# Kernel tuning notes

Measured on AMD Instinct MI355X. Metric: run time of the kernel, lower is better.

## Reference

```python
import jax, jax.numpy as jnp
import numpy as np

H, HS, C = 16, 64, 1024  # num_heads, head_size, n_embd

def setup_inputs() -> dict:
    key = jax.random.key(0)
    ks = jax.random.split(key, 5)
    B, T = 2, 2048
    s = 1.0 / np.sqrt(C)
    return {
        "x": jax.random.normal(ks[0], (B, T, C), dtype=jnp.float32),
        "Wq": jax.random.normal(ks[1], (H, C, HS), dtype=jnp.float32) * s,
        "Wk": jax.random.normal(ks[2], (H, C, HS), dtype=jnp.float32) * s,
        "Wv": jax.random.normal(ks[3], (H, C, HS), dtype=jnp.float32) * s,
        "Wo": jax.random.normal(ks[4], (C, C), dtype=jnp.float32) * s,
    }

def reference(x, Wq, Wk, Wv, Wo):
    B, T, Cdim = x.shape
    scale = Cdim ** -0.5  # original scales by n_embd**-0.5, not head_size
    q = jnp.einsum('btc,hcd->bhtd', x, Wq)
    k = jnp.einsum('btc,hcd->bhtd', x, Wk)
    v = jnp.einsum('btc,hcd->bhtd', x, Wv)
    wei = jnp.einsum('bhtd,bhsd->bhts', q, k) * scale  # [B,H,T,T]
    causal = jnp.tril(jnp.ones((T, T), dtype=bool))
    wei = jnp.where(causal, wei, -jnp.inf)
    wei = jax.nn.softmax(wei, axis=-1)
    out = jnp.einsum('bhts,bhsd->bhtd', wei, v)  # [B,H,T,HS]
    out = out.transpose(0, 2, 1, 3).reshape(B, T, -1)  # concat heads -> [B,T,C]
    return out @ Wo.T
```

## Files before the change

kernel.cpp:

```cpp
#include <hip/hip_runtime.h>

typedef unsigned short ushort_t;
typedef __bf16 bf16x8 __attribute__((ext_vector_type(8)));
typedef float f32x4 __attribute__((ext_vector_type(4)));
typedef float f32x16 __attribute__((ext_vector_type(16)));
typedef unsigned short ushortx8 __attribute__((ext_vector_type(8)));
typedef unsigned int uintx4 __attribute__((ext_vector_type(4)));

#define NH 16
#define HS 64
#define CD 1024
#define NB 2
#define NT 2048
#define BT (NB * NT)
#define N3 (3 * CD)

#define L2E_DIV32 0.04508422002778011f


__device__ __forceinline__ ushort_t bf16_rne(float f) {
  union { float f; unsigned u; } v; v.f = f;
  unsigned u = v.u;
  unsigned r = (u + 0x7FFFu + ((u >> 16) & 1u)) >> 16;
  return (ushort_t)r;
}

__device__ __forceinline__ void gload_lds16(const ushort_t* g, ushort_t* l) {
  __builtin_amdgcn_global_load_lds(
      (const __attribute__((address_space(1))) unsigned int*)g,
      (__attribute__((address_space(3))) unsigned int*)l, 16, 0, 0);
}

__device__ __forceinline__ f32x4 mfma16(ushortx8 a, ushortx8 b, f32x4 c) {
  return __builtin_amdgcn_mfma_f32_16x16x32_bf16(
      __builtin_bit_cast(bf16x8, a), __builtin_bit_cast(bf16x8, b), c, 0, 0, 0);
}

__device__ __forceinline__ f32x16 mfma32(ushortx8 a, ushortx8 b, f32x16 c) {
  return __builtin_amdgcn_mfma_f32_32x32x16_bf16(
      __builtin_bit_cast(bf16x8, a), __builtin_bit_cast(bf16x8, b), c, 0, 0, 0);
}

__device__ __forceinline__ unsigned cvt_pk_bf16(float lo, float hi) {
  unsigned r;
  asm("v_cvt_pk_bf16_f32 %0, %1, %2" : "=v"(r) : "v"(lo), "v"(hi));
  return r;
}

__device__ __forceinline__ void plswap(unsigned &a, unsigned &b) {
  asm volatile("v_permlane32_swap_b32 %0, %1" : "+v"(a), "+v"(b));
}


__global__ __launch_bounds__(256)
void pack_cast(const float4* __restrict__ in, ushort_t* __restrict__ out, int n4) {
  const int i = blockIdx.x * 256 + threadIdx.x;
  if (i >= n4) return;
  const float4 v = in[i];
  ushort4 r;
  r.x = bf16_rne(v.x); r.y = bf16_rne(v.y);
  r.z = bf16_rne(v.z); r.w = bf16_rne(v.w);
  *(ushort4*)(out + (size_t)i * 4) = r;
}

__global__ __launch_bounds__(256)
void pack_wqkv(const float* __restrict__ Wq, const float* __restrict__ Wk,
               const float* __restrict__ Wv, ushort_t* __restrict__ out) {
  __shared__ ushort_t tile[64 * 66];
  const int sh = blockIdx.y;
  const int s = sh >> 4, h = sh & 15;
  const float* W = (s == 0) ? Wq : ((s == 1) ? Wk : Wv);
  const int c0 = blockIdx.x * 64;
  const int t = threadIdx.x;
#pragma unroll
  for (int j = 0; j < 16; ++j) {
    const int idx = t + j * 256;
    const int ci = idx >> 6, d = idx & 63;
    const float v = W[(size_t)(h * 1024 + c0 + ci) * 64 + d];
    tile[d * 66 + ci] = bf16_rne(v);
  }
  __syncthreads();
#pragma unroll
  for (int j = 0; j < 16; ++j) {
    const int idx = t + j * 256;
    const int d = idx >> 6, ci = idx & 63;
    out[(size_t)(s * 1024 + h * 64 + d) * 1024 + c0 + ci] = tile[d * 66 + ci];
  }
}


template <bool OUT_BF16>
__global__ __launch_bounds__(256)
void gemm_bt(const ushort_t* __restrict__ A, const ushort_t* __restrict__ Bt,
             void* __restrict__ Cv, int M, int N, int K) {
  __shared__ __align__(16) ushort_t ldsA[2][128 * 32];
  __shared__ __align__(16) ushort_t ldsB[2][128 * 32];
  const int tid = threadIdx.x;
  const int lane = tid & 63;
  const int wave = tid >> 6;
  const int row0 = blockIdx.y * 128;
  const int col0 = blockIdx.x * 128;
  const int wm = wave >> 1, wn = wave & 1;

  f32x4 acc[4][4] = {};

  const int ce = (tid & 3) * 8;

  auto stage = [&](int buf, int kt) {
    const int kbase = kt * 32;
#pragma unroll
    for (int j = 0; j < 2; ++j) {
      const int r = j * 64 + (tid >> 2);
      gload_lds16(A + (size_t)(row0 + r) * K + kbase + ce,
                  &ldsA[buf][(j * 256 + wave * 64) * 8]);
      gload_lds16(Bt + (size_t)(col0 + r) * K + kbase + ce,
                  &ldsB[buf][(j * 256 + wave * 64) * 8]);
    }
  };

  const int arow_off = (wm * 64 + (lane & 15)) * 32 + (lane >> 4) * 8;
  const int brow_off = (wn * 64 + (lane & 15)) * 32 + (lane >> 4) * 8;

  auto compute = [&](int buf) {
    ushortx8 af[4], bf[4];
#pragma unroll
    for (int m = 0; m < 4; ++m)
      af[m] = *(const ushortx8*)&ldsA[buf][arow_off + m * 512];
#pragma unroll
    for (int n = 0; n < 4; ++n)
      bf[n] = *(const ushortx8*)&ldsB[buf][brow_off + n * 512];
#pragma unroll
    for (int m = 0; m < 4; ++m)
#pragma unroll
      for (int n = 0; n < 4; ++n)
        acc[m][n] = mfma16(af[m], bf[n], acc[m][n]);
  };

  stage(0, 0);
  __syncthreads();
  const int nk = K >> 5;
  for (int kt = 0; kt < nk; ++kt) {
    const int cur = kt & 1;
    if (kt + 1 < nk) stage(cur ^ 1, kt + 1);
    compute(cur);
    __syncthreads();
  }

#pragma unroll
  for (int m = 0; m < 4; ++m) {
    const int rbase = row0 + wm * 64 + m * 16 + (lane >> 4) * 4;
#pragma unroll
    for (int n = 0; n < 4; ++n) {
      const int col = col0 + wn * 64 + n * 16 + (lane & 15);
#pragma unroll
      for (int i = 0; i < 4; ++i) {
        const size_t off = (size_t)(rbase + i) * N + col;
        if constexpr (OUT_BF16) ((ushort_t*)Cv)[off] = bf16_rne(acc[m][n][i]);
        else                    ((float*)Cv)[off]    = acc[m][n][i];
      }
    }
  }
}


__global__ __launch_bounds__(256, 2)
void attn_fwd2(const ushort_t* __restrict__ QKV, ushort_t* __restrict__ O) {
  __shared__ __align__(16) ushort_t Klds[2][64 * 64];
  __shared__ __align__(16) ushort_t Vlds[2][64 * 64];

  const int tid = threadIdx.x;
  const int lane = tid & 63;
  const int w = tid >> 6;
  const int l31 = lane & 31;
  const int h = lane >> 5;

  const int d0 = blockIdx.x;
  const int bh = (d0 & 7) + 8 * (d0 >> 7);
  const int qb = 15 - ((d0 >> 3) & 15);
  const int b = bh >> 4, head = bh & 15;
  const size_t base = (size_t)b * NT * N3;

  const int qw0 = qb * 128 + w * 32;
  const int qg = qw0 + l31;
  const int ntiles = 2 * qb + 2;
  const int tmax = 2 * qb + (w >> 1);

  ushortx8 qf[4];
  {
    const ushort_t* qp = QKV + base + (size_t)qg * N3 + head * 64 + h * 8;
#pragma unroll
    for (int kc = 0; kc < 4; ++kc)
      qf[kc] = *(const ushortx8*)(qp + kc * 16);
  }

  f32x16 oA = {}, oB = {};
  float m_r = -INFINITY, l_r = 0.f;

  const int vr = l31;
  const int vc = w * 2 + h;

  ushortx8 vst0, vst1;
  {
    const ushort_t* vp = QKV + base + (size_t)(2 * vr) * N3 + 2048 + head * 64 + vc * 8;
    vst0 = *(const ushortx8*)(vp);
    vst1 = *(const ushortx8*)(vp + N3);
  }
#pragma unroll
  for (int i = 0; i < 2; ++i) {
    const int ch = i * 256 + tid;
    const int row = ch >> 3, cc = ch & 7;
    gload_lds16(QKV + base + (size_t)row * N3 + 1024 + head * 64 + ((cc ^ (row & 7)) * 8),
                &Klds[0][(i * 256 + w * 64) * 8]);
  }
#pragma unroll
  for (int e = 0; e < 8; ++e) {
    const int d = vc * 8 + e;
    ushort2 val; val.x = vst0[e]; val.y = vst1[e];
    *(ushort2*)((char*)&Vlds[0][0] + d * 128 + (((vr >> 2) ^ (d & 7)) * 16) + 4 * (vr & 3)) = val;
  }
  asm volatile("s_waitcnt lgkmcnt(0)" ::: "memory");

  int curb = 0;
  for (int t = 0; t < ntiles; ++t) {
    const bool hasn = (t + 1 < ntiles);
    const int nxt = curb ^ 1;
    if (hasn) {
      const int key0n = (t + 1) * 64;
      const ushort_t* vp =
          QKV + base + (size_t)(key0n + 2 * vr) * N3 + 2048 + head * 64 + vc * 8;
      vst0 = *(const ushortx8*)(vp);
      vst1 = *(const ushortx8*)(vp + N3);
#pragma unroll
      for (int i = 0; i < 2; ++i) {
        const int ch = i * 256 + tid;
        const int row = ch >> 3, cc = ch & 7;
        gload_lds16(QKV + base + (size_t)(key0n + row) * N3 + 1024 + head * 64 +
                        ((cc ^ (row & 7)) * 8),
                    &Klds[nxt][(i * 256 + w * 64) * 8]);
      }
      asm volatile("s_waitcnt vmcnt(4)" ::: "memory");
    } else {
      asm volatile("s_waitcnt vmcnt(0)" ::: "memory");
    }
    __builtin_amdgcn_s_barrier();
    asm volatile("" ::: "memory");

    if (t <= tmax) {
      const int key0 = t * 64;
      f32x16 sA = {}, sB = {};
#pragma unroll
      for (int kc = 0; kc < 4; ++kc) {
        const int cc0 = ((2 * kc + h) ^ (l31 & 7)) * 8;
        const ushortx8 k0 = *(const ushortx8*)&Klds[curb][l31 * 64 + cc0];
        const ushortx8 k1 = *(const ushortx8*)&Klds[curb][(32 + l31) * 64 + cc0];
        sA = mfma32(k0, qf[kc], sA);
        sB = mfma32(k1, qf[kc], sB);
      }

      float s[32];
#pragma unroll
      for (int r = 0; r < 16; ++r) {
        s[r]      = sA[r] * L2E_DIV32;
        s[16 + r] = sB[r] * L2E_DIV32;
      }
      if (key0 + 63 > qw0) {
        const int kb0 = key0 + 4 * h;
#pragma unroll
        for (int r = 0; r < 16; ++r) {
          const int krow = (r & 3) + 8 * (r >> 2);
          if (kb0 + krow > qg)      s[r]      = -INFINITY;
          if (kb0 + 32 + krow > qg) s[16 + r] = -INFINITY;
        }
      }

      float mx = s[0];
#pragma unroll
      for (int r = 1; r < 32; ++r) mx = fmaxf(mx, s[r]);
      mx = fmaxf(mx, __shfl_xor(mx, 32, 64));
      const float mn = fmaxf(m_r, mx);
      const float alpha = exp2f(m_r - mn);
      m_r = mn;
      float rs = 0.f;
#pragma unroll
      for (int r = 0; r < 32; ++r) {
        s[r] = exp2f(s[r] - mn);
        rs += s[r];
      }
      rs += __shfl_xor(rs, 32, 64);
      l_r = l_r * alpha + rs;
#pragma unroll
      for (int r = 0; r < 16; ++r) { oA[r] *= alpha; oB[r] *= alpha; }

      unsigned u[16];
#pragma unroll
      for (int j = 0; j < 16; ++j) u[j] = cvt_pk_bf16(s[2 * j], s[2 * j + 1]);
      plswap(u[0], u[2]);   plswap(u[1], u[3]);
      plswap(u[4], u[6]);   plswap(u[5], u[7]);
      plswap(u[8], u[10]);  plswap(u[9], u[11]);
      plswap(u[12], u[14]); plswap(u[13], u[15]);

#pragma unroll
      for (int kc = 0; kc < 4; ++kc) {
        uintx4 pw;
        pw[0] = u[4 * kc + 0]; pw[1] = u[4 * kc + 1];
        pw[2] = u[4 * kc + 2]; pw[3] = u[4 * kc + 3];
        const ushortx8 pav = __builtin_bit_cast(ushortx8, pw);
        const int cc0 = ((2 * kc + h) ^ (l31 & 7)) * 8;
        const ushortx8 va = *(const ushortx8*)&Vlds[curb][l31 * 64 + cc0];
        const ushortx8 vb = *(const ushortx8*)&Vlds[curb][(32 + l31) * 64 + cc0];
        oA = mfma32(va, pav, oA);
        oB = mfma32(vb, pav, oB);
      }
    }

    if (hasn) {
#pragma unroll
      for (int e = 0; e < 8; ++e) {
        const int d = vc * 8 + e;
        ushort2 val; val.x = vst0[e]; val.y = vst1[e];
        *(ushort2*)((char*)&Vlds[nxt][0] + d * 128 + (((vr >> 2) ^ (d & 7)) * 16) +
                    4 * (vr & 3)) = val;
      }
    }
    asm volatile("s_waitcnt lgkmcnt(0)" ::: "memory");
    __builtin_amdgcn_s_barrier();
    asm volatile("" ::: "memory");
    curb ^= 1;
  }

  const float inv_l = 1.0f / l_r;
  ushort_t* op = O + ((size_t)(b * NT + qg)) * 1024 + head * 64;
#pragma unroll
  for (int db = 0; db < 2; ++db) {
#pragma unroll
    for (int g = 0; g < 4; ++g) {
      ushort4 pk;
      if (db == 0) {
        pk.x = bf16_rne(oA[4 * g + 0] * inv_l);
        pk.y = bf16_rne(oA[4 * g + 1] * inv_l);
        pk.z = bf16_rne(oA[4 * g + 2] * inv_l);
        pk.w = bf16_rne(oA[4 * g + 3] * inv_l);
      } else {
        pk.x = bf16_rne(oB[4 * g + 0] * inv_l);
        pk.y = bf16_rne(oB[4 * g + 1] * inv_l);
        pk.z = bf16_rne(oB[4 * g + 2] * inv_l);
        pk.w = bf16_rne(oB[4 * g + 3] * inv_l);
      }
      *(ushort4*)(op + db * 32 + 8 * g + 4 * h) = pk;
    }
  }
}


extern "C" void kernel_launch(void* const* d_in, const int* in_sizes, int n_in,
                              void* d_out, int out_size, void* d_ws, size_t ws_size,
                              hipStream_t stream) {
  (void)in_sizes; (void)n_in; (void)out_size; (void)ws_size;
  const float* x  = (const float*)d_in[0];
  const float* Wq = (const float*)d_in[1];
  const float* Wk = (const float*)d_in[2];
  const float* Wv = (const float*)d_in[3];
  const float* Wo = (const float*)d_in[4];

  char* ws = (char*)d_ws;
  ushort_t* Xbf    = (ushort_t*)(ws);
  ushort_t* Wqkv_t = (ushort_t*)(ws + 8388608);
  ushort_t* Wo_bf  = (ushort_t*)(ws + 14680064);
  ushort_t* QKV    = (ushort_t*)(ws + 16777216);
  ushort_t* Obf    = (ushort_t*)(ws + 41943040);

  pack_cast<<<4096, 256, 0, stream>>>((const float4*)x, Xbf, 1048576);
  pack_cast<<<1024, 256, 0, stream>>>((const float4*)Wo, Wo_bf, 262144);
  pack_wqkv<<<dim3(16, 48), 256, 0, stream>>>(Wq, Wk, Wv, Wqkv_t);

  gemm_bt<true><<<dim3(24, 32), 256, 0, stream>>>(Xbf, Wqkv_t, QKV, BT, N3, CD);
  attn_fwd2<<<dim3(512), 256, 0, stream>>>(QKV, Obf);
  gemm_bt<false><<<dim3(8, 32), 256, 0, stream>>>(Obf, Wo_bf, d_out, BT, CD, CD);
}
```

Baseline: 148.0 us.

## Drop LDS staging in attention: pre-transpose V, load K/V directly into registers

Adds a separate kernel that transposes V into a head-major [d, T] layout so that attention waves can load V fragments straight from global memory. The attention kernel drops the shared-memory double buffer and block barriers. Each wave now handles its own 32-query tile and register-prefetches the next K tile, skips the fully masked half of the diagonal tile, and only rescales the accumulator when the running max grows by more than a threshold. The cost is an extra kernel launch and transpose pass, redundant global/L2 K/V reads across waves in place of shared LDS reuse, and higher register pressure.

```diff
diff --git a/kernel.cpp b/kernel.cpp
--- a/kernel.cpp
+++ b/kernel.cpp
@@ -85,6 +85,35 @@
     const int idx = t + j * 256;
     const int d = idx >> 6, ci = idx & 63;
     out[(size_t)(s * 1024 + h * 64 + d) * 1024 + c0 + ci] = tile[d * 66 + ci];
+  }
+}
+
+__global__ __launch_bounds__(256)
+void vtrans(const ushort_t* __restrict__ QKV, ushort_t* __restrict__ Vt) {
+  __shared__ ushort_t tile[64 * 66];
+  const int bh = blockIdx.y;
+  const int b = bh >> 4, h = bh & 15;
+  const int t0 = blockIdx.x * 64;
+  const int tid = threadIdx.x;
+  const ushort_t* src = QKV + ((size_t)b * NT + t0) * N3 + 2048 + h * 64;
+#pragma unroll
+  for (int i = 0; i < 2; ++i) {
+    const int ch = i * 256 + tid;
+    const int r = ch >> 3, c8 = ch & 7;
+    const ushortx8 v = *(const ushortx8*)(src + (size_t)r * N3 + c8 * 8);
+#pragma unroll
+    for (int e = 0; e < 8; ++e) tile[(c8 * 8 + e) * 66 + r] = v[e];
+  }
+  __syncthreads();
+  ushort_t* dst = Vt + ((size_t)bh * 64) * NT + t0;
+#pragma unroll
+  for (int i = 0; i < 2; ++i) {
+    const int ch = i * 256 + tid;
+    const int d = ch >> 3, c8 = ch & 7;
+    ushortx8 o;
+#pragma unroll
+    for (int e = 0; e < 8; ++e) o[e] = tile[d * 66 + c8 * 8 + e];
+    *(ushortx8*)(dst + (size_t)d * NT + c8 * 8) = o;
   }
 }
 
@@ -164,168 +193,179 @@
 
 
 __global__ __launch_bounds__(256, 2)
-void attn_fwd2(const ushort_t* __restrict__ QKV, ushort_t* __restrict__ O) {
-  __shared__ __align__(16) ushort_t Klds[2][64 * 64];
-  __shared__ __align__(16) ushort_t Vlds[2][64 * 64];
-
+void attn_fwd3(const ushort_t* __restrict__ QKV, const ushort_t* __restrict__ Vt,
+               ushort_t* __restrict__ O) {
   const int tid = threadIdx.x;
+  const int w = tid >> 6;
   const int lane = tid & 63;
-  const int w = tid >> 6;
   const int l31 = lane & 31;
   const int h = lane >> 5;
 
-  const int d0 = blockIdx.x;
-  const int bh = (d0 & 7) + 8 * (d0 >> 7);
-  const int qb = 15 - ((d0 >> 3) & 15);
+  const int x = blockIdx.x;
+  const int bh = x & 31;
+  const int qt = (15 - (x >> 5)) * 4 + w;
   const int b = bh >> 4, head = bh & 15;
   const size_t base = (size_t)b * NT * N3;
-
-  const int qw0 = qb * 128 + w * 32;
-  const int qg = qw0 + l31;
-  const int ntiles = 2 * qb + 2;
-  const int tmax = 2 * qb + (w >> 1);
+  const int q0 = qt * 32;
+  const int qg = q0 + l31;
+  const int ntiles = (qt >> 1) + 1;
+  const bool oddq = (qt & 1) != 0;
+
+  const ushort_t* Kbase = QKV + base + 1024 + head * 64;
+  const ushort_t* Vbase = Vt + ((size_t)bh * 64) * NT;
 
   ushortx8 qf[4];
   {
     const ushort_t* qp = QKV + base + (size_t)qg * N3 + head * 64 + h * 8;
 #pragma unroll
-    for (int kc = 0; kc < 4; ++kc)
-      qf[kc] = *(const ushortx8*)(qp + kc * 16);
+    for (int kc = 0; kc < 4; ++kc) qf[kc] = *(const ushortx8*)(qp + kc * 16);
   }
 
   f32x16 oA = {}, oB = {};
   float m_r = -INFINITY, l_r = 0.f;
 
-  const int vr = l31;
-  const int vc = w * 2 + h;
-
-  ushortx8 vst0, vst1;
+  ushortx8 ka0[4], ka1[4], kb0[4], kb1[4];
+
   {
-    const ushort_t* vp = QKV + base + (size_t)(2 * vr) * N3 + 2048 + head * 64 + vc * 8;
-    vst0 = *(const ushortx8*)(vp);
-    vst1 = *(const ushortx8*)(vp + N3);
-  }
-#pragma unroll
-  for (int i = 0; i < 2; ++i) {
-    const int ch = i * 256 + tid;
-    const int row = ch >> 3, cc = ch & 7;
-    gload_lds16(QKV + base + (size_t)row * N3 + 1024 + head * 64 + ((cc ^ (row & 7)) * 8),
-                &Klds[0][(i * 256 + w * 64) * 8]);
-  }
-#pragma unroll
-  for (int e = 0; e < 8; ++e) {
-    const int d = vc * 8 + e;
-    ushort2 val; val.x = vst0[e]; val.y = vst1[e];
-    *(ushort2*)((char*)&Vlds[0][0] + d * 128 + (((vr >> 2) ^ (d & 7)) * 16) + 4 * (vr & 3)) = val;
-  }
-  asm volatile("s_waitcnt lgkmcnt(0)" ::: "memory");
-
-  int curb = 0;
-  for (int t = 0; t < ntiles; ++t) {
-    const bool hasn = (t + 1 < ntiles);
-    const int nxt = curb ^ 1;
-    if (hasn) {
-      const int key0n = (t + 1) * 64;
-      const ushort_t* vp =
-          QKV + base + (size_t)(key0n + 2 * vr) * N3 + 2048 + head * 64 + vc * 8;
-      vst0 = *(const ushortx8*)(vp);
-      vst1 = *(const ushortx8*)(vp + N3);
-#pragma unroll
-      for (int i = 0; i < 2; ++i) {
-        const int ch = i * 256 + tid;
-        const int row = ch >> 3, cc = ch & 7;
-        gload_lds16(QKV + base + (size_t)(key0n + row) * N3 + 1024 + head * 64 +
-                        ((cc ^ (row & 7)) * 8),
-                    &Klds[nxt][(i * 256 + w * 64) * 8]);
-      }
-      asm volatile("s_waitcnt vmcnt(4)" ::: "memory");
-    } else {
-      asm volatile("s_waitcnt vmcnt(0)" ::: "memory");
-    }
-    __builtin_amdgcn_s_barrier();
-    asm volatile("" ::: "memory");
-
-    if (t <= tmax) {
-      const int key0 = t * 64;
-      f32x16 sA = {}, sB = {};
-#pragma unroll
-      for (int kc = 0; kc < 4; ++kc) {
-        const int cc0 = ((2 * kc + h) ^ (l31 & 7)) * 8;
-        const ushortx8 k0 = *(const ushortx8*)&Klds[curb][l31 * 64 + cc0];
-        const ushortx8 k1 = *(const ushortx8*)&Klds[curb][(32 + l31) * 64 + cc0];
-        sA = mfma32(k0, qf[kc], sA);
-        sB = mfma32(k1, qf[kc], sB);
-      }
-
-      float s[32];
-#pragma unroll
-      for (int r = 0; r < 16; ++r) {
-        s[r]      = sA[r] * L2E_DIV32;
-        s[16 + r] = sB[r] * L2E_DIV32;
-      }
-      if (key0 + 63 > qw0) {
-        const int kb0 = key0 + 4 * h;
+    const bool hB0 = (ntiles == 1) && !oddq;
+#pragma unroll
+    for (int kc = 0; kc < 4; ++kc)
+      ka0[kc] = *(const ushortx8*)(Kbase + (size_t)l31 * N3 + kc * 16 + h * 8);
+    if (!hB0) {
+#pragma unroll
+      for (int kc = 0; kc < 4; ++kc)
+        ka1[kc] = *(const ushortx8*)(Kbase + (size_t)(32 + l31) * N3 + kc * 16 + h * 8);
+    }
+  }
+
+  auto step = [&](int t, ushortx8 (&kc0)[4], ushortx8 (&kc1)[4],
+                  ushortx8 (&kn0)[4], ushortx8 (&kn1)[4]) {
+    const int key0 = t * 64;
+    const bool last = (t == ntiles - 1);
+    const bool halfB = last && !oddq;
+
+    ushortx8 va[4], vb[4];
+#pragma unroll
+    for (int kc = 0; kc < 4; ++kc) {
+      if (kc < 2 || !halfB) {
+        va[kc] = *(const ushortx8*)(Vbase + (size_t)l31 * NT + key0 + kc * 16 + h * 8);
+        vb[kc] = *(const ushortx8*)(Vbase + (size_t)(32 + l31) * NT + key0 + kc * 16 + h * 8);
+      }
+    }
+    if (t + 1 < ntiles) {
+      const int nk0 = (t + 1) * 64;
+      const bool nhB = (t + 1 == ntiles - 1) && !oddq;
+#pragma unroll
+      for (int kc = 0; kc < 4; ++kc)
+        kn0[kc] = *(const ushortx8*)(Kbase + (size_t)(nk0 + l31) * N3 + kc * 16 + h * 8);
+      if (!nhB) {
+#pragma unroll
+        for (int kc = 0; kc < 4; ++kc)
+          kn1[kc] = *(const ushortx8*)(Kbase + (size_t)(nk0 + 32 + l31) * N3 + kc * 16 + h * 8);
+      }
+    }
+
+    f32x16 sA = {}, sB = {};
+#pragma unroll
+    for (int kc = 0; kc < 4; ++kc) sA = mfma32(kc0[kc], qf[kc], sA);
+    if (!halfB) {
+#pragma unroll
+      for (int kc = 0; kc < 4; ++kc) sB = mfma32(kc1[kc], qf[kc], sB);
+    }
+
+#pragma unroll
+    for (int r = 0; r < 16; ++r) sA[r] *= L2E_DIV32;
+    if (!halfB) {
+#pragma unroll
+      for (int r = 0; r < 16; ++r) sB[r] *= L2E_DIV32;
+    }
+    if (last) {
+      const int kb = key0 + 4 * h;
+      if (halfB) {
 #pragma unroll
         for (int r = 0; r < 16; ++r) {
           const int krow = (r & 3) + 8 * (r >> 2);
-          if (kb0 + krow > qg)      s[r]      = -INFINITY;
-          if (kb0 + 32 + krow > qg) s[16 + r] = -INFINITY;
+          if (kb + krow > qg) sA[r] = -INFINITY;
         }
-      }
-
-      float mx = s[0];
-#pragma unroll
-      for (int r = 1; r < 32; ++r) mx = fmaxf(mx, s[r]);
-      mx = fmaxf(mx, __shfl_xor(mx, 32, 64));
+      } else {
+#pragma unroll
+        for (int r = 0; r < 16; ++r) {
+          const int krow = (r & 3) + 8 * (r >> 2);
+          if (kb + 32 + krow > qg) sB[r] = -INFINITY;
+        }
+      }
+    }
+
+    float mm[16];
+    if (!halfB) {
+#pragma unroll
+      for (int r = 0; r < 16; ++r) mm[r] = fmaxf(sA[r], sB[r]);
+    } else {
+#pragma unroll
+      for (int r = 0; r < 16; ++r) mm[r] = sA[r];
+    }
+#pragma unroll
+    for (int st = 8; st >= 1; st >>= 1)
+#pragma unroll
+      for (int r = 0; r < st; ++r) mm[r] = fmaxf(mm[r], mm[r + st]);
+    float mx = fmaxf(mm[0], __shfl_xor(mm[0], 32, 64));
+
+    if (__any(mx > m_r + 8.0f)) {
       const float mn = fmaxf(m_r, mx);
       const float alpha = exp2f(m_r - mn);
       m_r = mn;
-      float rs = 0.f;
-#pragma unroll
-      for (int r = 0; r < 32; ++r) {
-        s[r] = exp2f(s[r] - mn);
-        rs += s[r];
-      }
-      rs += __shfl_xor(rs, 32, 64);
-      l_r = l_r * alpha + rs;
+      l_r *= alpha;
 #pragma unroll
       for (int r = 0; r < 16; ++r) { oA[r] *= alpha; oB[r] *= alpha; }
-
-      unsigned u[16];
-#pragma unroll
-      for (int j = 0; j < 16; ++j) u[j] = cvt_pk_bf16(s[2 * j], s[2 * j + 1]);
-      plswap(u[0], u[2]);   plswap(u[1], u[3]);
-      plswap(u[4], u[6]);   plswap(u[5], u[7]);
+    }
+
+    unsigned u[16];
+    float ps[8];
+#pragma unroll
+    for (int j = 0; j < 8; ++j) {
+      const float e0 = exp2f(sA[2 * j] - m_r);
+      const float e1 = exp2f(sA[2 * j + 1] - m_r);
+      u[j] = cvt_pk_bf16(e0, e1);
+      ps[j] = e0 + e1;
+    }
+    if (!halfB) {
+#pragma unroll
+      for (int j = 0; j < 8; ++j) {
+        const float e0 = exp2f(sB[2 * j] - m_r);
+        const float e1 = exp2f(sB[2 * j + 1] - m_r);
+        u[8 + j] = cvt_pk_bf16(e0, e1);
+        ps[j] += e0 + e1;
+      }
+    }
+#pragma unroll
+    for (int st = 4; st >= 1; st >>= 1)
+#pragma unroll
+      for (int r = 0; r < st; ++r) ps[r] += ps[r + st];
+    l_r += ps[0] + __shfl_xor(ps[0], 32, 64);
+
+    plswap(u[0], u[2]);   plswap(u[1], u[3]);
+    plswap(u[4], u[6]);   plswap(u[5], u[7]);
+    if (!halfB) {
       plswap(u[8], u[10]);  plswap(u[9], u[11]);
       plswap(u[12], u[14]); plswap(u[13], u[15]);
-
-#pragma unroll
-      for (int kc = 0; kc < 4; ++kc) {
+    }
+
+#pragma unroll
+    for (int kc = 0; kc < 4; ++kc) {
+      if (kc < 2 || !halfB) {
         uintx4 pw;
         pw[0] = u[4 * kc + 0]; pw[1] = u[4 * kc + 1];
         pw[2] = u[4 * kc + 2]; pw[3] = u[4 * kc + 3];
         const ushortx8 pav = __builtin_bit_cast(ushortx8, pw);
-        const int cc0 = ((2 * kc + h) ^ (l31 & 7)) * 8;
-        const ushortx8 va = *(const ushortx8*)&Vlds[curb][l31 * 64 + cc0];
-        const ushortx8 vb = *(const ushortx8*)&Vlds[curb][(32 + l31) * 64 + cc0];
-        oA = mfma32(va, pav, oA);
-        oB = mfma32(vb, pav, oB);
-      }
-    }
-
-    if (hasn) {
-#pragma unroll
-      for (int e = 0; e < 8; ++e) {
-        const int d = vc * 8 + e;
-        ushort2 val; val.x = vst0[e]; val.y = vst1[e];
-        *(ushort2*)((char*)&Vlds[nxt][0] + d * 128 + (((vr >> 2) ^ (d & 7)) * 16) +
-                    4 * (vr & 3)) = val;
-      }
-    }
-    asm volatile("s_waitcnt lgkmcnt(0)" ::: "memory");
-    __builtin_amdgcn_s_barrier();
-    asm volatile("" ::: "memory");
-    curb ^= 1;
+        oA = mfma32(va[kc], pav, oA);
+        oB = mfma32(vb[kc], pav, oB);
+      }
+    }
+  };
+
+  for (int t = 0; t < ntiles; t += 2) {
+    step(t, ka0, ka1, kb0, kb1);
+    if (t + 1 < ntiles) step(t + 1, kb0, kb1, ka0, ka1);
   }
 
   const float inv_l = 1.0f / l_r;
@@ -368,12 +408,14 @@
   ushort_t* Wo_bf  = (ushort_t*)(ws + 14680064);
   ushort_t* QKV    = (ushort_t*)(ws + 16777216);
   ushort_t* Obf    = (ushort_t*)(ws + 41943040);
+  ushort_t* Vt     = (ushort_t*)(ws + 50331648);
 
   pack_cast<<<4096, 256, 0, stream>>>((const float4*)x, Xbf, 1048576);
   pack_cast<<<1024, 256, 0, stream>>>((const float4*)Wo, Wo_bf, 262144);
   pack_wqkv<<<dim3(16, 48), 256, 0, stream>>>(Wq, Wk, Wv, Wqkv_t);
 
   gemm_bt<true><<<dim3(24, 32), 256, 0, stream>>>(Xbf, Wqkv_t, QKV, BT, N3, CD);
-  attn_fwd2<<<dim3(512), 256, 0, stream>>>(QKV, Obf);
+  vtrans<<<dim3(32, 32), 256, 0, stream>>>(QKV, Vt);
+  attn_fwd3<<<512, 256, 0, stream>>>(QKV, Vt, Obf);
   gemm_bt<false><<<dim3(8, 32), 256, 0, stream>>>(Obf, Wo_bf, d_out, BT, CD, CD);
 }
```

New measurement: 164.7 us. 11.3% more time.

## Split long causal attention rows across blocks with a separate merge kernel

Applied to the files above, without the earlier changes.

Attention for long query blocks is split into 2 to 4 key-range chunks per block (split-KV), giving 1280 blocks with partial outputs and row max/sum stored in workspace. A new merge kernel then combines the chunks. Other changes: the softmax scale moves into the QKV GEMM epilogue, the diagonal tile skips its masked half, online-softmax rescaling only happens when the max grows by more than 8, and occupancy hints rise to 4 blocks. The cost is an extra launch, workspace traffic, and bf16 rounding of partial outputs.

```diff
diff --git a/kernel.cpp b/kernel.cpp
--- a/kernel.cpp
+++ b/kernel.cpp
@@ -17,12 +17,20 @@
 
 #define L2E_DIV32 0.04508422002778011f
 
+#define PART1_OFF 50331648
+#define SLOT_BYTES 18432
+#define R0_SLOTS 796
+
 
 __device__ __forceinline__ ushort_t bf16_rne(float f) {
   union { float f; unsigned u; } v; v.f = f;
   unsigned u = v.u;
   unsigned r = (u + 0x7FFFu + ((u >> 16) & 1u)) >> 16;
   return (ushort_t)r;
+}
+
+__device__ __forceinline__ float bf2f(ushort_t u) {
+  union { unsigned u; float f; } v; v.u = ((unsigned)u) << 16; return v.f;
 }
 
 __device__ __forceinline__ void gload_lds16(const ushort_t* g, ushort_t* l) {
@@ -92,7 +100,7 @@
 template <bool OUT_BF16>
 __global__ __launch_bounds__(256)
 void gemm_bt(const ushort_t* __restrict__ A, const ushort_t* __restrict__ Bt,
-             void* __restrict__ Cv, int M, int N, int K) {
+             void* __restrict__ Cv, int M, int N, int K, int qcols) {
   __shared__ __align__(16) ushort_t ldsA[2][128 * 32];
   __shared__ __align__(16) ushort_t ldsB[2][128 * 32];
   const int tid = threadIdx.x;
@@ -101,6 +109,7 @@
   const int row0 = blockIdx.y * 128;
   const int col0 = blockIdx.x * 128;
   const int wm = wave >> 1, wn = wave & 1;
+  const float sc = (col0 < qcols) ? L2E_DIV32 : 1.0f;
 
   f32x4 acc[4][4] = {};
 
@@ -122,18 +131,18 @@
   const int brow_off = (wn * 64 + (lane & 15)) * 32 + (lane >> 4) * 8;
 
   auto compute = [&](int buf) {
-    ushortx8 af[4], bf[4];
+    ushortx8 af[4], bfr[4];
 #pragma unroll
     for (int m = 0; m < 4; ++m)
       af[m] = *(const ushortx8*)&ldsA[buf][arow_off + m * 512];
 #pragma unroll
     for (int n = 0; n < 4; ++n)
-      bf[n] = *(const ushortx8*)&ldsB[buf][brow_off + n * 512];
+      bfr[n] = *(const ushortx8*)&ldsB[buf][brow_off + n * 512];
 #pragma unroll
     for (int m = 0; m < 4; ++m)
 #pragma unroll
       for (int n = 0; n < 4; ++n)
-        acc[m][n] = mfma16(af[m], bf[n], acc[m][n]);
+        acc[m][n] = mfma16(af[m], bfr[n], acc[m][n]);
   };
 
   stage(0, 0);
@@ -155,16 +164,17 @@
 #pragma unroll
       for (int i = 0; i < 4; ++i) {
         const size_t off = (size_t)(rbase + i) * N + col;
-        if constexpr (OUT_BF16) ((ushort_t*)Cv)[off] = bf16_rne(acc[m][n][i]);
-        else                    ((float*)Cv)[off]    = acc[m][n][i];
-      }
-    }
-  }
-}
-
-
-__global__ __launch_bounds__(256, 2)
-void attn_fwd2(const ushort_t* __restrict__ QKV, ushort_t* __restrict__ O) {
+        if constexpr (OUT_BF16) ((ushort_t*)Cv)[off] = bf16_rne(acc[m][n][i] * sc);
+        else                    ((float*)Cv)[off]    = acc[m][n][i] * sc;
+      }
+    }
+  }
+}
+
+
+__global__ __launch_bounds__(256, 4)
+void attn_fwd4(const ushort_t* __restrict__ QKV, ushort_t* __restrict__ O,
+               char* __restrict__ wsb) {
   __shared__ __align__(16) ushort_t Klds[2][64 * 64];
   __shared__ __align__(16) ushort_t Vlds[2][64 * 64];
 
@@ -174,70 +184,76 @@
   const int l31 = lane & 31;
   const int h = lane >> 5;
 
-  const int d0 = blockIdx.x;
-  const int bh = (d0 & 7) + 8 * (d0 >> 7);
-  const int qb = 15 - ((d0 >> 3) & 15);
+  const int x = blockIdx.x;
+  const int bh = x & 31;
+  const int c = x >> 5;
+  int qb, j, k;
+  if (c < 16)      { qb = 12 + (c >> 2); j = c & 3; k = 4; }
+  else if (c < 28) { const int e = c - 16; const int q = e / 3; qb = 8 + q; j = e - q * 3; k = 3; }
+  else if (c < 36) { const int e = c - 28; qb = 4 + (e >> 1); j = e & 1; k = 2; }
+  else             { qb = c - 36; j = 0; k = 1; }
+  const int nt = 2 * qb + 2;
+  const int bsz = nt / k, rem = nt - bsz * k;
+  const int t0 = j * bsz + (j < rem ? j : rem);
+  const int t1 = t0 + bsz + (j < rem ? 1 : 0);
+  const bool lastc = (t1 == nt);
+
   const int b = bh >> 4, head = bh & 15;
   const size_t base = (size_t)b * NT * N3;
-
   const int qw0 = qb * 128 + w * 32;
   const int qg = qw0 + l31;
-  const int ntiles = 2 * qb + 2;
-  const int tmax = 2 * qb + (w >> 1);
+  const int tmax = lastc ? (2 * qb + (w >> 1)) : (t1 - 1);
 
   ushortx8 qf[4];
   {
     const ushort_t* qp = QKV + base + (size_t)qg * N3 + head * 64 + h * 8;
 #pragma unroll
-    for (int kc = 0; kc < 4; ++kc)
-      qf[kc] = *(const ushortx8*)(qp + kc * 16);
-  }
+    for (int kc = 0; kc < 4; ++kc) qf[kc] = *(const ushortx8*)(qp + kc * 16);
+  }
+
+  int koff[4];
+#pragma unroll
+  for (int kc = 0; kc < 4; ++kc)
+    koff[kc] = l31 * 128 + (((2 * kc + h) ^ (l31 & 7)) * 16);
+
+  const int vr = l31, vc = w * 2 + h;
+  int voff[8];
+#pragma unroll
+  for (int e = 0; e < 8; ++e)
+    voff[e] = (vc * 8 + e) * 128 + (((vr >> 2) ^ e) * 16) + 4 * (vr & 3);
+
+  const int rowA = tid >> 3, ccA = tid & 7;
+  const int rowB = 32 + rowA;
+  const ushort_t* kg = QKV + base + 1024 + head * 64;
+  const ushort_t* ksA = kg + (size_t)(t0 * 64 + rowA) * N3 + ((ccA ^ (rowA & 7)) * 8);
+  const ushort_t* ksB = kg + (size_t)(t0 * 64 + rowB) * N3 + ((ccA ^ (rowB & 7)) * 8);
+  const ushort_t* vs  = QKV + base + (size_t)(t0 * 64 + 2 * vr) * N3 + 2048 + head * 64 + vc * 8;
+  const size_t tadv = (size_t)64 * N3;
 
   f32x16 oA = {}, oB = {};
   float m_r = -INFINITY, l_r = 0.f;
 
-  const int vr = l31;
-  const int vc = w * 2 + h;
-
-  ushortx8 vst0, vst1;
-  {
-    const ushort_t* vp = QKV + base + (size_t)(2 * vr) * N3 + 2048 + head * 64 + vc * 8;
-    vst0 = *(const ushortx8*)(vp);
-    vst1 = *(const ushortx8*)(vp + N3);
-  }
-#pragma unroll
-  for (int i = 0; i < 2; ++i) {
-    const int ch = i * 256 + tid;
-    const int row = ch >> 3, cc = ch & 7;
-    gload_lds16(QKV + base + (size_t)row * N3 + 1024 + head * 64 + ((cc ^ (row & 7)) * 8),
-                &Klds[0][(i * 256 + w * 64) * 8]);
-  }
+  ushortx8 vst0 = *(const ushortx8*)vs;
+  ushortx8 vst1 = *(const ushortx8*)(vs + N3);
+  gload_lds16(ksA, &Klds[0][(w * 64) * 8]);
+  gload_lds16(ksB, &Klds[0][(256 + w * 64) * 8]);
 #pragma unroll
   for (int e = 0; e < 8; ++e) {
-    const int d = vc * 8 + e;
     ushort2 val; val.x = vst0[e]; val.y = vst1[e];
-    *(ushort2*)((char*)&Vlds[0][0] + d * 128 + (((vr >> 2) ^ (d & 7)) * 16) + 4 * (vr & 3)) = val;
+    *(ushort2*)((char*)&Vlds[0][0] + voff[e]) = val;
   }
   asm volatile("s_waitcnt lgkmcnt(0)" ::: "memory");
 
   int curb = 0;
-  for (int t = 0; t < ntiles; ++t) {
-    const bool hasn = (t + 1 < ntiles);
+  for (int t = t0; t < t1; ++t) {
+    const bool hasn = (t + 1 < t1);
     const int nxt = curb ^ 1;
     if (hasn) {
-      const int key0n = (t + 1) * 64;
-      const ushort_t* vp =
-          QKV + base + (size_t)(key0n + 2 * vr) * N3 + 2048 + head * 64 + vc * 8;
-      vst0 = *(const ushortx8*)(vp);
-      vst1 = *(const ushortx8*)(vp + N3);
-#pragma unroll
-      for (int i = 0; i < 2; ++i) {
-        const int ch = i * 256 + tid;
-        const int row = ch >> 3, cc = ch & 7;
-        gload_lds16(QKV + base + (size_t)(key0n + row) * N3 + 1024 + head * 64 +
-                        ((cc ^ (row & 7)) * 8),
-                    &Klds[nxt][(i * 256 + w * 64) * 8]);
-      }
+      ksA += tadv; ksB += tadv; vs += tadv;
+      vst0 = *(const ushortx8*)vs;
+      vst1 = *(const ushortx8*)(vs + N3);
+      gload_lds16(ksA, &Klds[nxt][(w * 64) * 8]);
+      gload_lds16(ksB, &Klds[nxt][(256 + w * 64) * 8]);
       asm volatile("s_waitcnt vmcnt(4)" ::: "memory");
     } else {
       asm volatile("s_waitcnt vmcnt(0)" ::: "memory");
@@ -246,80 +262,96 @@
     asm volatile("" ::: "memory");
 
     if (t <= tmax) {
-      const int key0 = t * 64;
+      const bool diag = lastc && (t == tmax);
+      const bool halfB = diag && ((w & 1) == 0);
+      const char* kb = (const char*)&Klds[curb][0];
+      const char* vb = (const char*)&Vlds[curb][0];
+
       f32x16 sA = {}, sB = {};
 #pragma unroll
-      for (int kc = 0; kc < 4; ++kc) {
-        const int cc0 = ((2 * kc + h) ^ (l31 & 7)) * 8;
-        const ushortx8 k0 = *(const ushortx8*)&Klds[curb][l31 * 64 + cc0];
-        const ushortx8 k1 = *(const ushortx8*)&Klds[curb][(32 + l31) * 64 + cc0];
-        sA = mfma32(k0, qf[kc], sA);
-        sB = mfma32(k1, qf[kc], sB);
-      }
-
-      float s[32];
-#pragma unroll
-      for (int r = 0; r < 16; ++r) {
-        s[r]      = sA[r] * L2E_DIV32;
-        s[16 + r] = sB[r] * L2E_DIV32;
-      }
-      if (key0 + 63 > qw0) {
-        const int kb0 = key0 + 4 * h;
+      for (int kc = 0; kc < 4; ++kc)
+        sA = mfma32(*(const ushortx8*)(kb + koff[kc]), qf[kc], sA);
+      if (!halfB) {
+#pragma unroll
+        for (int kc = 0; kc < 4; ++kc)
+          sB = mfma32(*(const ushortx8*)(kb + 4096 + koff[kc]), qf[kc], sB);
+      }
+
+      if (diag) {
 #pragma unroll
         for (int r = 0; r < 16; ++r) {
-          const int krow = (r & 3) + 8 * (r >> 2);
-          if (kb0 + krow > qg)      s[r]      = -INFINITY;
-          if (kb0 + 32 + krow > qg) s[16 + r] = -INFINITY;
+          const int krow = (r & 3) + 8 * (r >> 2) + 4 * h;
+          if (halfB) { if (krow > l31) sA[r] = -INFINITY; }
+          else       { if (krow > l31) sB[r] = -INFINITY; }
         }
       }
 
-      float mx = s[0];
-#pragma unroll
-      for (int r = 1; r < 32; ++r) mx = fmaxf(mx, s[r]);
-      mx = fmaxf(mx, __shfl_xor(mx, 32, 64));
-      const float mn = fmaxf(m_r, mx);
-      const float alpha = exp2f(m_r - mn);
-      m_r = mn;
-      float rs = 0.f;
-#pragma unroll
-      for (int r = 0; r < 32; ++r) {
-        s[r] = exp2f(s[r] - mn);
-        rs += s[r];
-      }
-      rs += __shfl_xor(rs, 32, 64);
-      l_r = l_r * alpha + rs;
-#pragma unroll
-      for (int r = 0; r < 16; ++r) { oA[r] *= alpha; oB[r] *= alpha; }
+      float mm[16];
+#pragma unroll
+      for (int r = 0; r < 16; ++r) mm[r] = halfB ? sA[r] : fmaxf(sA[r], sB[r]);
+#pragma unroll
+      for (int st = 8; st >= 1; st >>= 1)
+#pragma unroll
+        for (int r = 0; r < st; ++r) mm[r] = fmaxf(mm[r], mm[r + st]);
+      const float mx = fmaxf(mm[0], __shfl_xor(mm[0], 32, 64));
+
+      if (__any(mx > m_r + 8.0f)) {
+        const float mn = fmaxf(m_r, mx);
+        const float al = exp2f(m_r - mn);
+        m_r = mn; l_r *= al;
+#pragma unroll
+        for (int r = 0; r < 16; ++r) { oA[r] *= al; oB[r] *= al; }
+      }
 
       unsigned u[16];
-#pragma unroll
-      for (int j = 0; j < 16; ++j) u[j] = cvt_pk_bf16(s[2 * j], s[2 * j + 1]);
+      float ps[8];
+#pragma unroll
+      for (int jj = 0; jj < 8; ++jj) {
+        const float e0 = exp2f(sA[2 * jj] - m_r);
+        const float e1 = exp2f(sA[2 * jj + 1] - m_r);
+        u[jj] = cvt_pk_bf16(e0, e1);
+        ps[jj] = e0 + e1;
+      }
+      if (!halfB) {
+#pragma unroll
+        for (int jj = 0; jj < 8; ++jj) {
+          const float e0 = exp2f(sB[2 * jj] - m_r);
+          const float e1 = exp2f(sB[2 * jj + 1] - m_r);
+          u[8 + jj] = cvt_pk_bf16(e0, e1);
+          ps[jj] += e0 + e1;
+        }
+      }
+#pragma unroll
+      for (int st = 4; st >= 1; st >>= 1)
+#pragma unroll
+        for (int r = 0; r < st; ++r) ps[r] += ps[r + st];
+      l_r += ps[0] + __shfl_xor(ps[0], 32, 64);
+
       plswap(u[0], u[2]);   plswap(u[1], u[3]);
       plswap(u[4], u[6]);   plswap(u[5], u[7]);
-      plswap(u[8], u[10]);  plswap(u[9], u[11]);
-      plswap(u[12], u[14]); plswap(u[13], u[15]);
+      if (!halfB) {
+        plswap(u[8], u[10]);  plswap(u[9], u[11]);
+        plswap(u[12], u[14]); plswap(u[13], u[15]);
+      }
 
 #pragma unroll
       for (int kc = 0; kc < 4; ++kc) {
-        uintx4 pw;
-        pw[0] = u[4 * kc + 0]; pw[1] = u[4 * kc + 1];
-        pw[2] = u[4 * kc + 2]; pw[3] = u[4 * kc + 3];
-        const ushortx8 pav = __builtin_bit_cast(ushortx8, pw);
-        const int cc0 = ((2 * kc + h) ^ (l31 & 7)) * 8;
-        const ushortx8 va = *(const ushortx8*)&Vlds[curb][l31 * 64 + cc0];
-        const ushortx8 vb = *(const ushortx8*)&Vlds[curb][(32 + l31) * 64 + cc0];
-        oA = mfma32(va, pav, oA);
-        oB = mfma32(vb, pav, oB);
+        if (kc < 2 || !halfB) {
+          uintx4 pw;
+          pw[0] = u[4 * kc + 0]; pw[1] = u[4 * kc + 1];
+          pw[2] = u[4 * kc + 2]; pw[3] = u[4 * kc + 3];
+          const ushortx8 pav = __builtin_bit_cast(ushortx8, pw);
+          oA = mfma32(*(const ushortx8*)(vb + koff[kc]), pav, oA);
+          oB = mfma32(*(const ushortx8*)(vb + 4096 + koff[kc]), pav, oB);
+        }
       }
     }
 
     if (hasn) {
 #pragma unroll
       for (int e = 0; e < 8; ++e) {
-        const int d = vc * 8 + e;
         ushort2 val; val.x = vst0[e]; val.y = vst1[e];
-        *(ushort2*)((char*)&Vlds[nxt][0] + d * 128 + (((vr >> 2) ^ (d & 7)) * 16) +
-                    4 * (vr & 3)) = val;
+        *(ushort2*)((char*)&Vlds[nxt][0] + voff[e]) = val;
       }
     }
     asm volatile("s_waitcnt lgkmcnt(0)" ::: "memory");
@@ -328,27 +360,103 @@
     curb ^= 1;
   }
 
-  const float inv_l = 1.0f / l_r;
+  if (k == 1) {
+    const float inv_l = 1.0f / l_r;
+    ushort_t* op = O + ((size_t)(b * NT + qg)) * 1024 + head * 64;
+#pragma unroll
+    for (int db = 0; db < 2; ++db)
+#pragma unroll
+      for (int g = 0; g < 4; ++g) {
+        ushort4 pk;
+        pk.x = bf16_rne((db ? oB[4 * g + 0] : oA[4 * g + 0]) * inv_l);
+        pk.y = bf16_rne((db ? oB[4 * g + 1] : oA[4 * g + 1]) * inv_l);
+        pk.z = bf16_rne((db ? oB[4 * g + 2] : oA[4 * g + 2]) * inv_l);
+        pk.w = bf16_rne((db ? oB[4 * g + 3] : oA[4 * g + 3]) * inv_l);
+        *(ushort4*)(op + db * 32 + 8 * g + 4 * h) = pk;
+      }
+  } else {
+    const int local = (qb < 8) ? ((qb - 4) * 2 + j)
+                    : (qb < 12) ? (8 + (qb - 8) * 3 + j)
+                    : (20 + (qb - 12) * 4 + j);
+    const int s = bh * 36 + local;
+    char* wb = (s < R0_SLOTS ? wsb + (size_t)s * SLOT_BYTES
+                             : wsb + PART1_OFF + (size_t)(s - R0_SLOTS) * SLOT_BYTES)
+               + w * 4608;
+#pragma unroll
+    for (int g = 0; g < 4; ++g) {
+      ushortx8 pk;
+#pragma unroll
+      for (int e2 = 0; e2 < 8; ++e2)
+        pk[e2] = bf16_rne(g < 2 ? oA[g * 8 + e2] : oB[(g - 2) * 8 + e2]);
+      *(ushortx8*)(wb + lane * 64 + g * 16) = pk;
+    }
+    *(float*)(wb + 4096 + lane * 4) = m_r;
+    *(float*)(wb + 4352 + lane * 4) = l_r;
+  }
+}
+
+__global__ __launch_bounds__(256)
+void attn_merge(const char* __restrict__ wsb, ushort_t* __restrict__ O) {
+  const int x = blockIdx.x;
+  const int bh = x & 31;
+  const int qi = x >> 5;
+  const int qb = 4 + qi;
+  const int k  = qi < 4 ? 2 : (qi < 8 ? 3 : 4);
+  const int lb = qi < 4 ? qi * 2 : (qi < 8 ? 8 + (qi - 4) * 3 : 20 + (qi - 8) * 4);
+  const int tid = threadIdx.x;
+  const int lane = tid & 63;
+  const int w = tid >> 6;
+  const int l31 = lane & 31;
+  const int h = lane >> 5;
+
+  const char* wbs[4];
+  float mj[4], lj[4];
+  float M = -INFINITY;
+#pragma unroll
+  for (int jj = 0; jj < 4; ++jj) {
+    if (jj < k) {
+      const int s = bh * 36 + lb + jj;
+      const char* wb = (s < R0_SLOTS ? wsb + (size_t)s * SLOT_BYTES
+                                     : wsb + PART1_OFF + (size_t)(s - R0_SLOTS) * SLOT_BYTES)
+                       + w * 4608;
+      wbs[jj] = wb;
+      mj[jj] = *(const float*)(wb + 4096 + lane * 4);
+      lj[jj] = *(const float*)(wb + 4352 + lane * 4);
+      M = fmaxf(M, mj[jj]);
+    }
+  }
+  float o[32];
+#pragma unroll
+  for (int r = 0; r < 32; ++r) o[r] = 0.f;
+  float lacc = 0.f;
+#pragma unroll
+  for (int jj = 0; jj < 4; ++jj) {
+    if (jj < k) {
+      const float a = exp2f(mj[jj] - M);
+      lacc += a * lj[jj];
+#pragma unroll
+      for (int g = 0; g < 4; ++g) {
+        const ushortx8 v = *(const ushortx8*)(wbs[jj] + lane * 64 + g * 16);
+#pragma unroll
+        for (int e = 0; e < 8; ++e) o[g * 8 + e] += a * bf2f(v[e]);
+      }
+    }
+  }
+  const float inv_l = 1.0f / lacc;
+  const int b = bh >> 4, head = bh & 15;
+  const int qg = qb * 128 + w * 32 + l31;
   ushort_t* op = O + ((size_t)(b * NT + qg)) * 1024 + head * 64;
 #pragma unroll
-  for (int db = 0; db < 2; ++db) {
+  for (int db = 0; db < 2; ++db)
 #pragma unroll
     for (int g = 0; g < 4; ++g) {
       ushort4 pk;
-      if (db == 0) {
-        pk.x = bf16_rne(oA[4 * g + 0] * inv_l);
-        pk.y = bf16_rne(oA[4 * g + 1] * inv_l);
-        pk.z = bf16_rne(oA[4 * g + 2] * inv_l);
-        pk.w = bf16_rne(oA[4 * g + 3] * inv_l);
-      } else {
-        pk.x = bf16_rne(oB[4 * g + 0] * inv_l);
-        pk.y = bf16_rne(oB[4 * g + 1] * inv_l);
-        pk.z = bf16_rne(oB[4 * g + 2] * inv_l);
-        pk.w = bf16_rne(oB[4 * g + 3] * inv_l);
-      }
+      pk.x = bf16_rne(o[db * 16 + 4 * g + 0] * inv_l);
+      pk.y = bf16_rne(o[db * 16 + 4 * g + 1] * inv_l);
+      pk.z = bf16_rne(o[db * 16 + 4 * g + 2] * inv_l);
+      pk.w = bf16_rne(o[db * 16 + 4 * g + 3] * inv_l);
       *(ushort4*)(op + db * 32 + 8 * g + 4 * h) = pk;
     }
-  }
 }
 
 
@@ -373,7 +481,8 @@
   pack_cast<<<1024, 256, 0, stream>>>((const float4*)Wo, Wo_bf, 262144);
   pack_wqkv<<<dim3(16, 48), 256, 0, stream>>>(Wq, Wk, Wv, Wqkv_t);
 
-  gemm_bt<true><<<dim3(24, 32), 256, 0, stream>>>(Xbf, Wqkv_t, QKV, BT, N3, CD);
-  attn_fwd2<<<dim3(512), 256, 0, stream>>>(QKV, Obf);
-  gemm_bt<false><<<dim3(8, 32), 256, 0, stream>>>(Obf, Wo_bf, d_out, BT, CD, CD);
-}
+  gemm_bt<true><<<dim3(24, 32), 256, 0, stream>>>(Xbf, Wqkv_t, QKV, BT, N3, CD, 1024);
+  attn_fwd4<<<1280, 256, 0, stream>>>(QKV, Obf, ws);
+  attn_merge<<<384, 256, 0, stream>>>(ws, Obf);
+  gemm_bt<false><<<dim3(8, 32), 256, 0, stream>>>(Obf, Wo_bf, d_out, BT, CD, CD, 0);
+}
```

After: 147.7 us. Within noise of the previous version (-0.1%).
